# Performance work log

Measured on AMD Instinct MI355X. Metric: run time of the kernel, lower is better.

Reference implementation:

```python
import jax, jax.numpy as jnp
import numpy as np

B, T, IN, H, L, OUT = 64, 512, 128, 256, 3, 50
G = 3 * H  # gate dim (r,z,n)


def setup_inputs() -> dict:
    key = jax.random.key(0)
    ks = jax.random.split(key, 18)
    s = 0.08  # keep gates out of saturation
    r = jax.random.normal
    return {
        "x": r(ks[0], (B, T, IN), jnp.float32),
        "Wih0": r(ks[1], (2, G, IN)) * s,
        "Whh0": r(ks[2], (2, G, H)) * s,
        "bih0": r(ks[3], (2, G)) * s,
        "bhh0": r(ks[4], (2, G)) * s,
        "Wih": r(ks[5], (L - 1, 2, G, 2 * H)) * s,
        "Whh": r(ks[6], (L - 1, 2, G, H)) * s,
        "bih": r(ks[7], (L - 1, 2, G)) * s,
        "bhh": r(ks[8], (L - 1, 2, G)) * s,
        "W1": r(ks[9], (128, 2 * H)) * s,
        "b1": r(ks[10], (128,)) * s,
        "W2": r(ks[11], (64, 128)) * s,
        "b2": r(ks[12], (64,)) * s,
        "W3": r(ks[13], (H, 64)) * s,
        "b3": r(ks[14], (H,)) * s,
        "W4": r(ks[15], (OUT, H)) * s,
        "b4": r(ks[16], (OUT,)) * s,
    }


def _gru_dir(x, Wih, Whh, bih, bhh, reverse):
    # x: [B,T,D]. Precompute input gates with one big GEMM, scan only hidden matmul.
    xg = jnp.einsum('btd,gd->tbg', x, Wih) + bih  # [T,B,3H]
    h0 = jnp.zeros((x.shape[0], H), x.dtype)

    def step(h, xg_t):
        hg = h @ Whh.T + bhh                     # [B,3H]
        xr, xz, xn = jnp.split(xg_t, 3, axis=-1)
        hr, hz, hn = jnp.split(hg, 3, axis=-1)
        r = jax.nn.sigmoid(xr + hr)
        z = jax.nn.sigmoid(xz + hz)
        n = jnp.tanh(xn + r * hn)
        h = (1.0 - z) * n + z * h
        return h, h

    _, ys = jax.lax.scan(step, h0, xg, reverse=reverse)  # ys[t] aligned to time t
    return jnp.transpose(ys, (1, 0, 2))  # [B,T,H]


def reference(x, Wih0, Whh0, bih0, bhh0, Wih, Whh, bih, bhh,
              W1, b1, W2, b2, W3, b3, W4, b4):
    h = x
    for l in range(L):
        if l == 0:
            wi, wh, bi, bh = Wih0, Whh0, bih0, bhh0
        else:
            wi, wh, bi, bh = Wih[l - 1], Whh[l - 1], bih[l - 1], bhh[l - 1]
        fwd = _gru_dir(h, wi[0], wh[0], bi[0], bh[0], False)
        bwd = _gru_dir(h, wi[1], wh[1], bi[1], bh[1], True)
        h = jnp.concatenate([fwd, bwd], axis=-1)  # [B,T,2H]
    last = h[:, -1, :]  # [B,2H]
    y = jax.nn.relu(last @ W1.T + b1)
    y = jax.nn.relu(y @ W2.T + b2)
    y = jax.nn.relu(y @ W3.T + b3)
    return y @ W4.T + b4  # [B,OUT]
```

## Files before the change

### kernel.cpp

```cpp
#include <hip/hip_runtime.h>
#include <stdint.h>

#define B_ 64
#define T_ 512
#define IN_ 128
#define H_ 256
#define G_ 768
#define M0_ (B_*T_)

typedef _Float16 f16;
typedef _Float16 f16x2 __attribute__((ext_vector_type(2)));
typedef _Float16 half8 __attribute__((ext_vector_type(8)));
typedef float f32x4 __attribute__((ext_vector_type(4)));

#if __has_builtin(__builtin_amdgcn_fdot2)
__device__ inline float fdot2f(f16x2 a, f16x2 b, float c){ return __builtin_amdgcn_fdot2(a, b, c, false); }
#else
__device__ inline float fdot2f(f16x2 a, f16x2 b, float c){ return c + (float)a.x*(float)b.x + (float)a.y*(float)b.y; }
#endif

template<bool AF32>
__global__ __launch_bounds__(256) void k_proj(
    const float* __restrict__ Af, const f16* __restrict__ Ah,
    const float* __restrict__ W, const float* __restrict__ bias,
    f16* __restrict__ out, int K)
{
  int dir = blockIdx.z;
  const float* Wd = W + (size_t)dir*G_*K;
  const float* bd = bias + dir*G_;
  f16* outd = out + (size_t)dir*M0_*G_;
  int m0 = blockIdx.x*128, n0 = blockIdx.y*128;
  int tid = threadIdx.x, lane = tid & 63, wv = tid >> 6;
  int wm = wv >> 1, wn = wv & 1;
  int l15 = lane & 15, quad = lane >> 4;

  __shared__ f16 As[128][72];
  __shared__ f16 Ws[128][72];

  f32x4 acc[4][4];
  #pragma unroll
  for (int i = 0; i < 4; i++)
    #pragma unroll
    for (int j = 0; j < 4; j++) acc[i][j] = (f32x4){0.f,0.f,0.f,0.f};

  int lr = tid >> 3, lk = (tid & 7) * 8;
  for (int k0 = 0; k0 < K; k0 += 64){
    #pragma unroll
    for (int it = 0; it < 4; it++){
      int row = lr + it*32;
      if (AF32){
        const float* p = &Af[(size_t)(m0+row)*K + k0 + lk];
        float4 v0 = *(const float4*)p;
        float4 v1 = *(const float4*)(p + 4);
        *(half8*)&As[row][lk] = (half8){(f16)v0.x,(f16)v0.y,(f16)v0.z,(f16)v0.w,
                                        (f16)v1.x,(f16)v1.y,(f16)v1.z,(f16)v1.w};
      } else {
        *(uint4*)&As[row][lk] = *(const uint4*)&Ah[(size_t)(m0+row)*K + k0 + lk];
      }
      {
        const float* p = &Wd[(size_t)(n0+row)*K + k0 + lk];
        float4 v0 = *(const float4*)p;
        float4 v1 = *(const float4*)(p + 4);
        *(half8*)&Ws[row][lk] = (half8){(f16)v0.x,(f16)v0.y,(f16)v0.z,(f16)v0.w,
                                        (f16)v1.x,(f16)v1.y,(f16)v1.z,(f16)v1.w};
      }
    }
    __syncthreads();
    #pragma unroll
    for (int kk = 0; kk < 64; kk += 32){
      half8 af[4], bf[4];
      #pragma unroll
      for (int mi = 0; mi < 4; mi++) af[mi] = *(const half8*)&As[wm*64 + mi*16 + l15][kk + quad*8];
      #pragma unroll
      for (int ni = 0; ni < 4; ni++) bf[ni] = *(const half8*)&Ws[wn*64 + ni*16 + l15][kk + quad*8];
      #pragma unroll
      for (int mi = 0; mi < 4; mi++)
        #pragma unroll
        for (int ni = 0; ni < 4; ni++)
          acc[mi][ni] = __builtin_amdgcn_mfma_f32_16x16x32_f16(af[mi], bf[ni], acc[mi][ni], 0, 0, 0);
    }
    __syncthreads();
  }
  #pragma unroll
  for (int mi = 0; mi < 4; mi++){
    #pragma unroll
    for (int ni = 0; ni < 4; ni++){
      int m = m0 + wm*64 + mi*16 + quad*4;
      int n = n0 + wn*64 + ni*16 + l15;
      float bn = bd[n];
      #pragma unroll
      for (int r = 0; r < 4; r++)
        outd[(size_t)(m+r)*G_ + n] = (f16)(acc[mi][ni][r] + bn);
    }
  }
}

__global__ __launch_bounds__(512) __attribute__((amdgpu_waves_per_eu(2, 2)))
void k_rnn(
    const f16* __restrict__ xg, const float* __restrict__ whh,
    const float* __restrict__ bhh, f16* __restrict__ y)
{
  int b = blockIdx.x, dir = blockIdx.y;
  int tid = threadIdx.x, lane = tid & 63, wv = tid >> 6;
  int g = lane >> 4;
  int i = lane & 15;
  int o = lane & 31;
  int u = wv*32 + o;
  int dsel = (lane >> 4) & 1;

  const f16* cxg = xg + ((size_t)dir*M0_ + (size_t)b*T_)*G_;
  const float* wbase = whh + (size_t)dir*G_*H_;
  const float* bh = bhh + dir*G_;
  f16* yb = y + (size_t)b*T_*512 + dir*256;

  __shared__ __align__(16) f16 h0buf[256];
  __shared__ __align__(16) f16 h1buf[256];

  f16x2 wf2[192];
  #pragma unroll
  for (int m = 0; m < 6; m++){
    int gamma = m >> 1, d = m & 1;
    const float* wrow = wbase + (size_t)(gamma*256 + wv*32 + i + d*16)*H_ + g*64;
    #pragma unroll
    for (int q = 0; q < 16; q++){
      float4 v = ((const float4*)wrow)[q];
      wf2[m*32 + q*2 + 0] = (f16x2){(f16)v.x, (f16)v.y};
      wf2[m*32 + q*2 + 1] = (f16x2){(f16)v.z, (f16)v.w};
    }
  }

  float br = bh[u], bz = bh[u+256], bn = bh[u+512];
  float hreg = 0.f;
  if (tid < 256) h0buf[tid] = (f16)0.f;
  __syncthreads();

  f16 axr, axz, axn, bxr, bxz, bxn;
  {
    int t0 = dir ? (T_-1) : 0;
    const f16* xp = cxg + (size_t)t0*G_ + u;
    axr = xp[0]; axz = xp[256]; axn = xp[512];
  }

#define RSTEP(SRC, DST, XR, XZ, XN, TT)                                         \
  {                                                                             \
    const half8* hp = (const half8*)&SRC[g*64];                                 \
    half8 hv[8];                                                                \
    _Pragma("unroll")                                                           \
    for (int s2 = 0; s2 < 8; s2++) hv[s2] = hp[s2];                             \
    float ac[6] = {0.f,0.f,0.f,0.f,0.f,0.f};                                    \
    _Pragma("unroll")                                                           \
    for (int s2 = 0; s2 < 8; s2++){                                             \
      half8 hh = hv[s2];                                                        \
      _Pragma("unroll")                                                         \
      for (int q = 0; q < 4; q++){                                              \
        f16x2 pp = {hh[2*q], hh[2*q+1]};                                        \
        _Pragma("unroll")                                                       \
        for (int m = 0; m < 6; m++)                                             \
          ac[m] = fdot2f(wf2[m*32 + s2*4 + q], pp, ac[m]);                      \
      }                                                                         \
    }                                                                           \
    _Pragma("unroll")                                                           \
    for (int m = 0; m < 6; m++){                                                \
      ac[m] += __shfl_xor(ac[m], 16);                                           \
      ac[m] += __shfl_xor(ac[m], 32);                                           \
    }                                                                           \
    float sr = dsel ? ac[1] : ac[0];                                            \
    float sz = dsel ? ac[3] : ac[2];                                            \
    float sn = dsel ? ac[5] : ac[4];                                            \
    float ar = (float)(XR) + sr + br; ar = fminf(fmaxf(ar, -30.f), 30.f);       \
    float az = (float)(XZ) + sz + bz; az = fminf(fmaxf(az, -30.f), 30.f);       \
    float r_ = 1.f/(1.f + __expf(-ar));                                         \
    float z_ = 1.f/(1.f + __expf(-az));                                         \
    float an = (float)(XN) + r_*(sn + bn); an = fminf(fmaxf(an, -15.f), 15.f);  \
    float e_ = __expf(2.f*an);                                                  \
    float nn = (e_ - 1.f)/(e_ + 1.f);                                           \
    hreg = (1.f - z_)*nn + z_*hreg;                                             \
    if (lane < 32){                                                             \
      DST[u] = (f16)hreg;                                                       \
      yb[(size_t)(TT)*512 + u] = (f16)hreg;                                     \
    }                                                                           \
    asm volatile("s_waitcnt lgkmcnt(0)\n\ts_barrier" ::: "memory");             \
  }

  for (int s = 0; s < T_; s += 2){
    int ttA = dir ? (T_-1-s) : s;
    int ttB = dir ? (T_-2-s) : (s+1);

    {
      const f16* xq = cxg + (size_t)ttB*G_ + u;
      bxr = xq[0]; bxz = xq[256]; bxn = xq[512];
    }
    RSTEP(h0buf, h1buf, axr, axz, axn, ttA)

    {
      int s2c = (s + 2 < T_) ? (s + 2) : (T_ - 1);
      int tt2 = dir ? (T_-1-s2c) : s2c;
      const f16* xq = cxg + (size_t)tt2*G_ + u;
      axr = xq[0]; axz = xq[256]; axn = xq[512];
    }
    RSTEP(h1buf, h0buf, bxr, bxz, bxn, ttB)
  }
#undef RSTEP
}

__global__ __launch_bounds__(256) void k_head(
    const f16* __restrict__ y,
    const float* __restrict__ W1, const float* __restrict__ b1,
    const float* __restrict__ W2, const float* __restrict__ b2,
    const float* __restrict__ W3, const float* __restrict__ b3,
    const float* __restrict__ W4, const float* __restrict__ b4,
    float* __restrict__ out)
{
  int b = blockIdx.x, tid = threadIdx.x;
  __shared__ float a0[512], a1[128], a2[64], a3[256];
  const f16* yr = y + ((size_t)b*T_ + (T_-1))*512;
  a0[tid] = (float)yr[tid]; a0[tid+256] = (float)yr[tid+256];
  __syncthreads();
  if (tid < 128){
    float s = b1[tid];
    const float4* w = (const float4*)(W1 + (size_t)tid*512);
    #pragma unroll 8
    for (int c = 0; c < 128; c++){
      float4 v = w[c];
      s += v.x*a0[c*4] + v.y*a0[c*4+1] + v.z*a0[c*4+2] + v.w*a0[c*4+3];
    }
    a1[tid] = fmaxf(s, 0.f);
  }
  __syncthreads();
  if (tid < 64){
    float s = b2[tid];
    const float4* w = (const float4*)(W2 + (size_t)tid*128);
    #pragma unroll
    for (int c = 0; c < 32; c++){
      float4 v = w[c];
      s += v.x*a1[c*4] + v.y*a1[c*4+1] + v.z*a1[c*4+2] + v.w*a1[c*4+3];
    }
    a2[tid] = fmaxf(s, 0.f);
  }
  __syncthreads();
  if (tid < 256){
    float s = b3[tid];
    const float4* w = (const float4*)(W3 + (size_t)tid*64);
    #pragma unroll
    for (int c = 0; c < 16; c++){
      float4 v = w[c];
      s += v.x*a2[c*4] + v.y*a2[c*4+1] + v.z*a2[c*4+2] + v.w*a2[c*4+3];
    }
    a3[tid] = fmaxf(s, 0.f);
  }
  __syncthreads();
  if (tid < 50){
    float s = b4[tid];
    const float4* w = (const float4*)(W4 + (size_t)tid*256);
    #pragma unroll
    for (int c = 0; c < 64; c++){
      float4 v = w[c];
      s += v.x*a3[c*4] + v.y*a3[c*4+1] + v.z*a3[c*4+2] + v.w*a3[c*4+3];
    }
    out[b*50 + tid] = s;
  }
}

extern "C" void kernel_launch(void* const* d_in, const int* in_sizes, int n_in,
                              void* d_out, int out_size, void* d_ws, size_t ws_size,
                              hipStream_t stream)
{
  const float* x    = (const float*)d_in[0];
  const float* Wih0 = (const float*)d_in[1];
  const float* Whh0 = (const float*)d_in[2];
  const float* bih0 = (const float*)d_in[3];
  const float* bhh0 = (const float*)d_in[4];
  const float* Wih  = (const float*)d_in[5];
  const float* Whh  = (const float*)d_in[6];
  const float* bih  = (const float*)d_in[7];
  const float* bhh  = (const float*)d_in[8];
  const float* W1 = (const float*)d_in[9];
  const float* b1 = (const float*)d_in[10];
  const float* W2 = (const float*)d_in[11];
  const float* b2 = (const float*)d_in[12];
  const float* W3 = (const float*)d_in[13];
  const float* b3 = (const float*)d_in[14];
  const float* W4 = (const float*)d_in[15];
  const float* b4 = (const float*)d_in[16];

  char* ws = (char*)d_ws;
  f16* xg = (f16*)ws;
  f16* y  = (f16*)(ws + 100663296ull);

  k_proj<true ><<<dim3(M0_/128, 6, 2), dim3(256), 0, stream>>>(x, nullptr, Wih0, bih0, xg, IN_);
  k_rnn        <<<dim3(B_, 2),         dim3(512), 0, stream>>>(xg, Whh0, bhh0, y);
  k_proj<false><<<dim3(M0_/128, 6, 2), dim3(256), 0, stream>>>(nullptr, y, Wih, bih, xg, 2*H_);
  k_rnn        <<<dim3(B_, 2),         dim3(512), 0, stream>>>(xg, Whh, bhh, y);
  k_proj<false><<<dim3(M0_/128, 6, 2), dim3(256), 0, stream>>>(nullptr, y, Wih + 1ull*2*G_*(2*H_), bih + 2*G_, xg, 2*H_);
  k_rnn        <<<dim3(B_, 2),         dim3(512), 0, stream>>>(xg, Whh + 1ull*2*G_*H_, bhh + 2*G_, y);

  k_head<<<dim3(B_), dim3(256), 0, stream>>>(y, W1, b1, W2, b2, W3, b3, W4, b4,
                                             (float*)d_out);
}
```

Before: 2.409 ms.

## Compute r/z recurrent gates with MFMA and keep n gate on fdot2

The recurrent hidden matmul for the r and z gates now uses 16x16x32 f16 MFMA instructions, with the weights held in registers as MFMA B-fragments and h broadcast as the A operand. The n gate stays on the scalar fdot2 path, split across two half-waves with a single shuffle reduction. The goal is to shorten the per-timestep serial latency of the dot products and cut shuffle reductions. In exchange, MFMA computes 16 rows of which only one is used, which wastes matrix work, and there is a risk of register pressure and lane-mapping errors.

```diff
diff --git a/kernel.cpp b/kernel.cpp
--- a/kernel.cpp
+++ b/kernel.cpp
@@ -102,11 +102,11 @@
 {
   int b = blockIdx.x, dir = blockIdx.y;
   int tid = threadIdx.x, lane = tid & 63, wv = tid >> 6;
-  int g = lane >> 4;
-  int i = lane & 15;
-  int o = lane & 31;
-  int u = wv*32 + o;
+  int col = lane & 15;
+  int kg  = lane >> 4;
+  int u   = wv*32 + (lane & 31);
   int dsel = (lane >> 4) & 1;
+  int half = lane >> 5;
 
   const f16* cxg = xg + ((size_t)dir*M0_ + (size_t)b*T_)*G_;
   const float* wbase = whh + (size_t)dir*G_*H_;
@@ -116,16 +116,28 @@
   __shared__ __align__(16) f16 h0buf[256];
   __shared__ __align__(16) f16 h1buf[256];
 
-  f16x2 wf2[192];
+  half8 wf[32];
   #pragma unroll
-  for (int m = 0; m < 6; m++){
-    int gamma = m >> 1, d = m & 1;
-    const float* wrow = wbase + (size_t)(gamma*256 + wv*32 + i + d*16)*H_ + g*64;
-    #pragma unroll
-    for (int q = 0; q < 16; q++){
+  for (int t = 0; t < 4; t++){
+    int g = t >> 1, c = t & 1;
+    const float* wrow = wbase + (size_t)(g*256 + wv*32 + c*16 + col)*H_;
+    #pragma unroll
+    for (int kf = 0; kf < 8; kf++){
+      const float4* p = (const float4*)(wrow + kf*32 + kg*8);
+      float4 v0 = p[0], v1 = p[1];
+      wf[t*8+kf] = (half8){(f16)v0.x,(f16)v0.y,(f16)v0.z,(f16)v0.w,
+                           (f16)v1.x,(f16)v1.y,(f16)v1.z,(f16)v1.w};
+    }
+  }
+
+  f16x2 wfn[64];
+  {
+    const float* wrow = wbase + (size_t)(512 + u)*H_ + half*128;
+    #pragma unroll
+    for (int q = 0; q < 32; q++){
       float4 v = ((const float4*)wrow)[q];
-      wf2[m*32 + q*2 + 0] = (f16x2){(f16)v.x, (f16)v.y};
-      wf2[m*32 + q*2 + 1] = (f16x2){(f16)v.z, (f16)v.w};
+      wfn[q*2 + 0] = (f16x2){(f16)v.x, (f16)v.y};
+      wfn[q*2 + 1] = (f16x2){(f16)v.z, (f16)v.w};
     }
   }
 
@@ -143,30 +155,45 @@
 
 #define RSTEP(SRC, DST, XR, XZ, XN, TT)                                         \
   {                                                                             \
-    const half8* hp = (const half8*)&SRC[g*64];                                 \
-    half8 hv[8];                                                                \
+    const f16* hp = &SRC[kg*8];               \
+    const half8* hq = (const half8*)&SRC[half*128];  \
+    f32x4 acc0, acc1, acc2, acc3;                                               \
+    float an0 = 0.f, an1 = 0.f;                                                 \
+    half8 acur = *(const half8*)hp;                                             \
+    half8 anxt = *(const half8*)(hp + 32);                                      \
     _Pragma("unroll")                                                           \
-    for (int s2 = 0; s2 < 8; s2++) hv[s2] = hp[s2];                             \
-    float ac[6] = {0.f,0.f,0.f,0.f,0.f,0.f};                                    \
-    _Pragma("unroll")                                                           \
-    for (int s2 = 0; s2 < 8; s2++){                                             \
-      half8 hh = hv[s2];                                                        \
+    for (int kf = 0; kf < 8; kf++){                                             \
+      half8 ac = acur;                                                          \
+      acur = anxt;                                                              \
+      if (kf < 6) anxt = *(const half8*)(hp + (kf+2)*32);                       \
+      half8 hh0 = hq[kf*2], hh1 = hq[kf*2+1];                                   \
+      if (kf == 0){                                                             \
+        acc0 = __builtin_amdgcn_mfma_f32_16x16x32_f16(ac, wf[0*8+kf],           \
+                 (f32x4){0.f,0.f,0.f,0.f}, 0, 0, 0);                            \
+        acc1 = __builtin_amdgcn_mfma_f32_16x16x32_f16(ac, wf[1*8+kf],           \
+                 (f32x4){0.f,0.f,0.f,0.f}, 0, 0, 0);                            \
+        acc2 = __builtin_amdgcn_mfma_f32_16x16x32_f16(ac, wf[2*8+kf],           \
+                 (f32x4){0.f,0.f,0.f,0.f}, 0, 0, 0);                            \
+        acc3 = __builtin_amdgcn_mfma_f32_16x16x32_f16(ac, wf[3*8+kf],           \
+                 (f32x4){0.f,0.f,0.f,0.f}, 0, 0, 0);                            \
+      } else {                                                                  \
+        acc0 = __builtin_amdgcn_mfma_f32_16x16x32_f16(ac, wf[0*8+kf], acc0, 0,0,0); \
+        acc1 = __builtin_amdgcn_mfma_f32_16x16x32_f16(ac, wf[1*8+kf], acc1, 0,0,0); \
+        acc2 = __builtin_amdgcn_mfma_f32_16x16x32_f16(ac, wf[2*8+kf], acc2, 0,0,0); \
+        acc3 = __builtin_amdgcn_mfma_f32_16x16x32_f16(ac, wf[3*8+kf], acc3, 0,0,0); \
+      }                                                                         \
       _Pragma("unroll")                                                         \
-      for (int q = 0; q < 4; q++){                                              \
-        f16x2 pp = {hh[2*q], hh[2*q+1]};                                        \
-        _Pragma("unroll")                                                       \
-        for (int m = 0; m < 6; m++)                                             \
-          ac[m] = fdot2f(wf2[m*32 + s2*4 + q], pp, ac[m]);                      \
+      for (int e = 0; e < 4; e++){                                              \
+        f16x2 p0 = {hh0[2*e], hh0[2*e+1]};                                      \
+        f16x2 p1 = {hh1[2*e], hh1[2*e+1]};                                      \
+        an0 = fdot2f(wfn[kf*8 + e],     p0, an0);                               \
+        an1 = fdot2f(wfn[kf*8 + 4 + e], p1, an1);                               \
       }                                                                         \
     }                                                                           \
-    _Pragma("unroll")                                                           \
-    for (int m = 0; m < 6; m++){                                                \
-      ac[m] += __shfl_xor(ac[m], 16);                                           \
-      ac[m] += __shfl_xor(ac[m], 32);                                           \
-    }                                                                           \
-    float sr = dsel ? ac[1] : ac[0];                                            \
-    float sz = dsel ? ac[3] : ac[2];                                            \
-    float sn = dsel ? ac[5] : ac[4];                                            \
+    float sn = an0 + an1;                                                       \
+    sn += __shfl_xor(sn, 32);                                                   \
+    float sr = dsel ? acc1[0] : acc0[0];                                        \
+    float sz = dsel ? acc3[0] : acc2[0];                                        \
     float ar = (float)(XR) + sr + br; ar = fminf(fmaxf(ar, -30.f), 30.f);       \
     float az = (float)(XZ) + sz + bz; az = fminf(fmaxf(az, -30.f), 30.f);       \
     float r_ = 1.f/(1.f + __expf(-ar));                                         \
```

Result: slower. 2.503 ms (+3.9%).
